# Kernel optimization log

Measured on AMD Instinct MI355X. Metric: run time of the kernel, lower is better.

## Reference

```python
import jax, jax.numpy as jnp
import numpy as np


def _patch_indices():
    # 36 positions (6x6 grid), each gathering a 3x3 window of 6-channel squares
    # from the flattened 385-vector: index = x*48 + y*6 + c
    idx = []
    for i in range(36):
        x, y = i // 6, i % 6
        rows = []
        for ox in range(3):
            for oy in range(3):
                base = (x + ox) * 48 + (y + oy) * 6
                rows.extend(range(base, base + 6))
        idx.append(rows)
    return jnp.asarray(np.array(idx, dtype=np.int32))  # [36, 54]


_IDX = _patch_indices()


def _crelu(v):
    return jnp.clip(v, -1.0, 1.0)


def setup_inputs() -> dict:
    key = jax.random.key(0)
    ks = jax.random.split(key, 13)
    B = 131072
    inp = jax.random.normal(ks[0], (B, 385), dtype=jnp.float32)
    s = 0.2  # small init scale
    # sight stack: 54 -> 8 -> 8 -> 1  (stored as [in, out])
    W1 = jax.random.normal(ks[1], (54, 8), jnp.float32) * s
    b1 = jax.random.normal(ks[2], (8,), jnp.float32) * s
    W2 = jax.random.normal(ks[3], (8, 8), jnp.float32) * s
    b2 = jax.random.normal(ks[4], (8,), jnp.float32) * s
    W3 = jax.random.normal(ks[5], (8, 1), jnp.float32) * s
    b3 = jax.random.normal(ks[6], (1,), jnp.float32) * s
    # evaluation stack: 37 -> 16 -> 16 -> 1
    E1 = jax.random.normal(ks[7], (37, 16), jnp.float32) * s
    c1 = jax.random.normal(ks[8], (16,), jnp.float32) * s
    E2 = jax.random.normal(ks[9], (16, 16), jnp.float32) * s
    c2 = jax.random.normal(ks[10], (16,), jnp.float32) * s
    E3 = jax.random.normal(ks[11], (16, 1), jnp.float32) * s
    c3 = jax.random.normal(ks[12], (1,), jnp.float32) * s
    return {"inp": inp, "W1": W1, "b1": b1, "W2": W2, "b2": b2,
            "W3": W3, "b3": b3, "E1": E1, "c1": c1, "E2": E2, "c2": c2,
            "E3": E3, "c3": c3}


def reference(inp, W1, b1, W2, b2, W3, b3, E1, c1, E2, c2, E3, c3):
    # inp: [B, 385]
    patches = inp[:, _IDX]                       # [B, 36, 54] windowed gather
    h = _crelu(jnp.einsum('bpf,fo->bpo', patches, W1) + b1)   # [B, 36, 8]
    h = _crelu(jnp.einsum('bpf,fo->bpo', h, W2) + b2)         # [B, 36, 8]
    v = _crelu(jnp.einsum('bpf,fo->bpo', h, W3) + b3)[..., 0]  # [B, 36]
    vision = jnp.concatenate([v, inp[:, 384:385]], axis=1)    # [B, 37]
    g = _crelu(vision @ E1 + c1)                 # [B, 16]
    g = _crelu(g @ E2 + c2)                      # [B, 16]
    out = _crelu(g @ E3 + c3)                    # [B, 1]
    return out
```

## Files before the change

kernel.cpp:

```cpp
#include <hip/hip_runtime.h>

typedef __attribute__((ext_vector_type(8))) short short8;
typedef __attribute__((ext_vector_type(4))) float float4v;

__device__ __forceinline__ float crelu(float v) {
    return fminf(1.0f, fmaxf(-1.0f, v));
}
__device__ __forceinline__ uint f2bf_u(float v) {
    uint u = __float_as_uint(v);
    u += 0x7fffu + ((u >> 16) & 1u);
    return u >> 16;
}
__device__ __forceinline__ ushort f2bf(float v) { return (ushort)f2bf_u(v); }

#define ROW 385
#define BT  16
#define BS  388

#define SLAB_BYTES 5440

__global__ __launch_bounds__(256, 7)
void lila_wave(const float* __restrict__ inp,
               const float* __restrict__ W1, const float* __restrict__ b1,
               const float* __restrict__ W2, const float* __restrict__ b2,
               const float* __restrict__ W3, const float* __restrict__ b3,
               const float* __restrict__ E1, const float* __restrict__ c1,
               const float* __restrict__ E2, const float* __restrict__ c2,
               const float* __restrict__ E3, const float* __restrict__ c3,
               float* __restrict__ out)
{
    __shared__ __align__(16) char slab_all[4 * SLAB_BYTES];

    const int tid  = threadIdx.x;
    const int lane = tid & 63;
    const int wv   = tid >> 6;
    const int quad = lane >> 4;
    const int nn   = lane & 15;
    const int m0   = quad * 8;

    char*   slab  = slab_all + wv * SLAB_BYTES;
    ushort* board = (ushort*)slab;
    ushort* hbuf  = (ushort*)(slab + 3136);
    float*  vis   = (float*)slab;
    float*  g1    = (float*)(slab + 640);

    const long long b0w = (long long)blockIdx.x * BT + wv * 4;

    short8 bfr[3];
    #pragma unroll
    for (int r = 0; r < 3; ++r) {
        #pragma unroll
        for (int j = 0; j < 8; ++j) {
            int k = m0 + j;
            float w = (k < 18 && nn < 8) ? W1[(r * 18 + k) * 8 + nn] : 0.0f;
            bfr[r][j] = (short)f2bf(w);
        }
    }
    const float bias1 = (nn < 8) ? b1[nn] : 0.0f;

    const int r   = lane >> 4;
    const int c16 = lane & 15;
    const float* gr = inp + (b0w + r) * ROW;

    if (lane < 4) *(unsigned long long*)(board + lane * BS + 384) = 0ULL;
    if (lane >= 4 && lane < 8)
        *(unsigned long long*)(slab + 3104 + (lane - 4) * 8) = 0ULL;

    #pragma unroll
    for (int j = 0; j < 12; ++j) {
        int e = 2 * (c16 + 16 * j);
        float f0 = gr[e], f1 = gr[e + 1];
        uint pk = f2bf_u(f0) | (f2bf_u(f1) << 16);
        *(uint*)((char*)board + r * 776 + 2 * e) = pk;
    }
    const float cen = gr[384];

    asm volatile("" ::: "memory");

    #pragma unroll 1
    for (int t = 0; t < 9; ++t) {
        int ltask = t * 16 + nn;
        uint lb = (uint)ltask / 36u;
        uint p  = (uint)ltask - 36u * lb;
        uint x  = p / 6u;
        uint y  = p - 6u * x;
        const uint* bp = (const uint*)(board + lb * BS + x * 48 + 6 * y + m0);
        union { uint u[4]; short8 s; } a0, a1, a2;
        #pragma unroll
        for (int q = 0; q < 4; ++q) {
            a0.u[q] = bp[q];
            a1.u[q] = bp[24 + q];
            a2.u[q] = bp[48 + q];
        }
        float4v acc = { bias1, bias1, bias1, bias1 };
        acc = __builtin_amdgcn_mfma_f32_16x16x32_bf16(a0.s, bfr[0], acc, 0, 0, 0);
        acc = __builtin_amdgcn_mfma_f32_16x16x32_bf16(a1.s, bfr[1], acc, 0, 0, 0);
        acc = __builtin_amdgcn_mfma_f32_16x16x32_bf16(a2.s, bfr[2], acc, 0, 0, 0);
        if (nn < 8) {
            #pragma unroll
            for (int i = 0; i < 4; ++i) {
                int trow = t * 16 + quad * 4 + i;
                hbuf[trow * 8 + nn] = f2bf(crelu(acc[i]));
            }
        }
    }

    asm volatile("" ::: "memory");

    #pragma unroll 1
    for (int it = 0; it < 3; ++it) {
        int task = lane + it * 64;
        if (task < 144) {
            uint lb = (uint)task / 36u;
            uint p  = (uint)task - 36u * lb;
            uint4 hv = *(const uint4*)(hbuf + task * 8);
            float h[8];
            h[0] = __uint_as_float(hv.x << 16);
            h[1] = __uint_as_float(hv.x & 0xffff0000u);
            h[2] = __uint_as_float(hv.y << 16);
            h[3] = __uint_as_float(hv.y & 0xffff0000u);
            h[4] = __uint_as_float(hv.z << 16);
            h[5] = __uint_as_float(hv.z & 0xffff0000u);
            h[6] = __uint_as_float(hv.w << 16);
            h[7] = __uint_as_float(hv.w & 0xffff0000u);

            float a2[8];
            #pragma unroll
            for (int o = 0; o < 8; ++o) a2[o] = b2[o];
            #pragma unroll
            for (int i = 0; i < 8; ++i) {
                #pragma unroll
                for (int o = 0; o < 8; ++o)
                    a2[o] = fmaf(h[i], W2[i * 8 + o], a2[o]);
            }
            float v = b3[0];
            #pragma unroll
            for (int i = 0; i < 8; ++i) v = fmaf(crelu(a2[i]), W3[i], v);
            vis[lb * 40 + p] = crelu(v);
        }
    }

    asm volatile("" ::: "memory");

    {
        const int o = nn;
        float a = c1[o];
        #pragma unroll
        for (int f = 0; f < 36; ++f)
            a = fmaf(vis[r * 40 + f], E1[f * 16 + o], a);
        a = fmaf(cen, E1[36 * 16 + o], a);
        g1[r * 17 + o] = crelu(a);

        asm volatile("" ::: "memory");

        float a2 = c2[o];
        #pragma unroll
        for (int f = 0; f < 16; ++f)
            a2 = fmaf(g1[r * 17 + f], E2[f * 16 + o], a2);
        float t = crelu(a2) * E3[o];
        t += __shfl_xor(t, 1);
        t += __shfl_xor(t, 2);
        t += __shfl_xor(t, 4);
        t += __shfl_xor(t, 8);
        if (o == 0) out[b0w + r] = crelu(t + c3[0]);
    }
}

extern "C" void kernel_launch(void* const* d_in, const int* in_sizes, int n_in,
                              void* d_out, int out_size, void* d_ws, size_t ws_size,
                              hipStream_t stream)
{
    const float* inp = (const float*)d_in[0];
    const float* W1  = (const float*)d_in[1];
    const float* b1  = (const float*)d_in[2];
    const float* W2  = (const float*)d_in[3];
    const float* b2  = (const float*)d_in[4];
    const float* W3  = (const float*)d_in[5];
    const float* b3  = (const float*)d_in[6];
    const float* E1  = (const float*)d_in[7];
    const float* c1  = (const float*)d_in[8];
    const float* E2  = (const float*)d_in[9];
    const float* c2  = (const float*)d_in[10];
    const float* E3  = (const float*)d_in[11];
    const float* c3  = (const float*)d_in[12];
    float* out = (float*)d_out;

    int B = in_sizes[0] / ROW;
    int grid = B / BT;
    lila_wave<<<grid, 256, 0, stream>>>(inp, W1, b1, W2, b2, W3, b3,
                                        E1, c1, E2, c2, E3, c3, out);
}
```

Baseline: 300.5 us.

## Pad board cells to 8 channels for 16-byte LDS loads in the MFMA stage

Each 6-channel board square is now stored as 8 bf16 values in LDS, with zero padding, so each MFMA A-fragment comes from one aligned uint4 load instead of four 32-bit loads. W1 fragments are remapped to match the padded channel layout. Global reads become float2 loads per cell, and the E1/E2 dot products now read vis and g1 with float4 LDS loads. In exchange the per-wave slab grows, and the occupancy hint drops from 7 to 6 blocks per CU.

Result: no change. 298.9 us (-0.6%).

```diff
diff --git a/kernel.cpp b/kernel.cpp
--- a/kernel.cpp
+++ b/kernel.cpp
@@ -15,11 +15,10 @@
 
 #define ROW 385
 #define BT  16
-#define BS  388
-
-#define SLAB_BYTES 5440
-
-__global__ __launch_bounds__(256, 7)
+
+#define SLAB_BYTES 6656
+
+__global__ __launch_bounds__(256, 6)
 void lila_wave(const float* __restrict__ inp,
                const float* __restrict__ W1, const float* __restrict__ b1,
                const float* __restrict__ W2, const float* __restrict__ b2,
@@ -40,7 +39,7 @@
 
     char*   slab  = slab_all + wv * SLAB_BYTES;
     ushort* board = (ushort*)slab;
-    ushort* hbuf  = (ushort*)(slab + 3136);
+    ushort* hbuf  = (ushort*)(slab + 4352);
     float*  vis   = (float*)slab;
     float*  g1    = (float*)(slab + 640);
 
@@ -51,8 +50,9 @@
     for (int r = 0; r < 3; ++r) {
         #pragma unroll
         for (int j = 0; j < 8; ++j) {
-            int k = m0 + j;
-            float w = (k < 18 && nn < 8) ? W1[(r * 18 + k) * 8 + nn] : 0.0f;
+            int k = m0 + j, oy = k >> 3, c = k & 7;
+            float w = (oy < 3 && c < 6 && nn < 8)
+                    ? W1[(r * 18 + oy * 6 + c) * 8 + nn] : 0.0f;
             bfr[r][j] = (short)f2bf(w);
         }
     }
@@ -62,16 +62,24 @@
     const int c16 = lane & 15;
     const float* gr = inp + (b0w + r) * ROW;
 
-    if (lane < 4) *(unsigned long long*)(board + lane * BS + 384) = 0ULL;
-    if (lane >= 4 && lane < 8)
-        *(unsigned long long*)(slab + 3104 + (lane - 4) * 8) = 0ULL;
-
+    if (c16 < 4) {
+        uint4 z = {0u, 0u, 0u, 0u};
+        *(uint4*)(board + r * 544 + 512 + c16 * 8) = z;
+    }
     #pragma unroll
-    for (int j = 0; j < 12; ++j) {
-        int e = 2 * (c16 + 16 * j);
-        float f0 = gr[e], f1 = gr[e + 1];
-        uint pk = f2bf_u(f0) | (f2bf_u(f1) << 16);
-        *(uint*)((char*)board + r * 776 + 2 * e) = pk;
+    for (int u = 0; u < 4; ++u) {
+        int cell = c16 + 16 * u;
+        int X = cell >> 3, Y = cell & 7;
+        int g = X * 48 + Y * 6;
+        float2 p0 = *(const float2*)(gr + g);
+        float2 p1 = *(const float2*)(gr + g + 2);
+        float2 p2 = *(const float2*)(gr + g + 4);
+        uint4 pk;
+        pk.x = f2bf_u(p0.x) | (f2bf_u(p0.y) << 16);
+        pk.y = f2bf_u(p1.x) | (f2bf_u(p1.y) << 16);
+        pk.z = f2bf_u(p2.x) | (f2bf_u(p2.y) << 16);
+        pk.w = 0u;
+        *(uint4*)(board + r * 544 + cell * 8) = pk;
     }
     const float cen = gr[384];
 
@@ -84,24 +92,19 @@
         uint p  = (uint)ltask - 36u * lb;
         uint x  = p / 6u;
         uint y  = p - 6u * x;
-        const uint* bp = (const uint*)(board + lb * BS + x * 48 + 6 * y + m0);
-        union { uint u[4]; short8 s; } a0, a1, a2;
-        #pragma unroll
-        for (int q = 0; q < 4; ++q) {
-            a0.u[q] = bp[q];
-            a1.u[q] = bp[24 + q];
-            a2.u[q] = bp[48 + q];
-        }
+        const ushort* base = board + lb * 544 + x * 64 + 8 * y + m0;
+        union { uint4 u; short8 s; } a0, a1, a2;
+        a0.u = *(const uint4*)(base);
+        a1.u = *(const uint4*)(base + 64);
+        a2.u = *(const uint4*)(base + 128);
         float4v acc = { bias1, bias1, bias1, bias1 };
         acc = __builtin_amdgcn_mfma_f32_16x16x32_bf16(a0.s, bfr[0], acc, 0, 0, 0);
         acc = __builtin_amdgcn_mfma_f32_16x16x32_bf16(a1.s, bfr[1], acc, 0, 0, 0);
         acc = __builtin_amdgcn_mfma_f32_16x16x32_bf16(a2.s, bfr[2], acc, 0, 0, 0);
         if (nn < 8) {
             #pragma unroll
-            for (int i = 0; i < 4; ++i) {
-                int trow = t * 16 + quad * 4 + i;
-                hbuf[trow * 8 + nn] = f2bf(crelu(acc[i]));
-            }
+            for (int i = 0; i < 4; ++i)
+                hbuf[(t * 16 + quad * 4 + i) * 8 + nn] = f2bf(crelu(acc[i]));
         }
     }
 
@@ -146,23 +149,33 @@
         const int o = nn;
         float a = c1[o];
         #pragma unroll
-        for (int f = 0; f < 36; ++f)
-            a = fmaf(vis[r * 40 + f], E1[f * 16 + o], a);
+        for (int fi = 0; fi < 9; ++fi) {
+            float4 vv = *(const float4*)(vis + r * 40 + fi * 4);
+            a = fmaf(vv.x, E1[(fi * 4 + 0) * 16 + o], a);
+            a = fmaf(vv.y, E1[(fi * 4 + 1) * 16 + o], a);
+            a = fmaf(vv.z, E1[(fi * 4 + 2) * 16 + o], a);
+            a = fmaf(vv.w, E1[(fi * 4 + 3) * 16 + o], a);
+        }
         a = fmaf(cen, E1[36 * 16 + o], a);
-        g1[r * 17 + o] = crelu(a);
+        g1[r * 20 + o] = crelu(a);
 
         asm volatile("" ::: "memory");
 
         float a2 = c2[o];
         #pragma unroll
-        for (int f = 0; f < 16; ++f)
-            a2 = fmaf(g1[r * 17 + f], E2[f * 16 + o], a2);
-        float t = crelu(a2) * E3[o];
-        t += __shfl_xor(t, 1);
-        t += __shfl_xor(t, 2);
-        t += __shfl_xor(t, 4);
-        t += __shfl_xor(t, 8);
-        if (o == 0) out[b0w + r] = crelu(t + c3[0]);
+        for (int fi = 0; fi < 4; ++fi) {
+            float4 gv = *(const float4*)(g1 + r * 20 + fi * 4);
+            a2 = fmaf(gv.x, E2[(fi * 4 + 0) * 16 + o], a2);
+            a2 = fmaf(gv.y, E2[(fi * 4 + 1) * 16 + o], a2);
+            a2 = fmaf(gv.z, E2[(fi * 4 + 2) * 16 + o], a2);
+            a2 = fmaf(gv.w, E2[(fi * 4 + 3) * 16 + o], a2);
+        }
+        float tv = crelu(a2) * E3[o];
+        tv += __shfl_xor(tv, 1);
+        tv += __shfl_xor(tv, 2);
+        tv += __shfl_xor(tv, 4);
+        tv += __shfl_xor(tv, 8);
+        if (o == 0) out[b0w + r] = crelu(tv + c3[0]);
     }
 }
 
```
